# Kernel optimization log

Hardware: AMD Instinct MI355X
Metric: run time of the kernel (lower is better)

Reference implementation:

```python
import jax, jax.numpy as jnp
import numpy as np

EPS = 1e-9
TOP_K = 2


def setup_inputs() -> dict:
    key = jax.random.key(0)
    k = jax.random.split(key, 6)
    B, E, D_IN, D_MODEL, D_SEL = 16384, 8, 900, 512, 128
    return {
        "cycle_curve_data": jax.random.normal(k[0], (B, D_IN), jnp.float32),
        "logits": jax.random.normal(k[1], (B, E), jnp.float32),
        "moe_masks": jax.random.randint(k[2], (B, E), 0, 2, jnp.int32),
        "selection_embeddings": jax.random.normal(k[3], (B, E, D_SEL), jnp.float32),
        "W": jax.random.normal(k[4], (E, D_IN, D_MODEL), jnp.float32) / np.sqrt(D_IN).astype(np.float32),
        "b": jnp.zeros((E, D_MODEL), jnp.float32),
    }


def reference(cycle_curve_data, logits, moe_masks, selection_embeddings, W, b):
    B, E = logits.shape
    mask = (moe_masks == 1).astype(logits.dtype)  # [B, E]
    raw = jax.nn.softmax(logits, axis=1)          # [B, E]

    # inactive-expert mixture for selection embedding
    inactive = raw * (1.0 - mask)
    inactive = inactive / (jnp.sum(inactive, axis=1, keepdims=True) + EPS)
    selection_embedding = jnp.einsum("bes,be->bs", selection_embeddings, inactive)

    # active gates + top-k selection + renormalization
    active = raw * mask
    _, idx = jax.lax.top_k(active, TOP_K)                                  # [B, K]
    top_mask = jnp.sum(jax.nn.one_hot(idx, E, dtype=active.dtype), axis=1)  # [B, E]
    gates = active * top_mask
    gates = gates / (jnp.sum(gates, axis=1, keepdims=True) + EPS)

    # dense formulation of dispatch -> per-expert Linear -> weighted combine:
    # out[b] = sum_e gates[b,e] * (x[b] @ W[e] + b[e])
    expert_out = jnp.einsum("bd,edm->bem", cycle_curve_data, W) + b  # [B, E, D_model]
    final_out = jnp.einsum("bem,be->bm", expert_out, gates).astype(jnp.bfloat16)

    # guide loss (training-mode auxiliary loss)
    s = jnp.sum(raw * mask) / B
    guide_loss = (1.0 - s) * (1.0 - s)
    return final_out, guide_loss, selection_embedding
```

## Files before the change

kernel.cpp:

```cpp
#include <hip/hip_runtime.h>
#include <hip/hip_bf16.h>


#define B_ROWS 16384
#define DIN 900
#define DM 512
#define DSEL 128
#define KP 928
#define NKS 29
#define MAXT 192
#define EPSF 1e-9f

#define OUT_GUIDE (B_ROWS*DM)
#define OUT_SEL   (B_ROWS*DM + 1)

#define WS_COUNTS 0
#define WS_PART   512
#define WS_NT     768
#define WS_OFF    1024
#define WS_ENT    2048
#define WS_BB     9216
#define WS_PIDLR  25600
#define WS_GATEB  91136
#define WS_W8     222208
#define WS_ROWSS  746496
#define WS_WT     812032

typedef __attribute__((ext_vector_type(8))) short short8;
typedef __attribute__((ext_vector_type(8))) unsigned short ushort8;
typedef __attribute__((ext_vector_type(4))) float floatx4;

__device__ inline unsigned short f2bf(float v){
  union { __hip_bfloat16 h; unsigned short u; } c;
  c.h = __float2bfloat16(v);
  return c.u;
}
__device__ inline float bf2f(unsigned short u){
  union { unsigned int i; float f; } c;
  c.i = ((unsigned int)u) << 16;
  return c.f;
}

__global__ __launch_bounds__(256) void cvtw_k(const float* __restrict__ W,
                                              unsigned short* __restrict__ wt){
  __shared__ unsigned short tl[64][65];
  int kt = blockIdx.x, ntb = blockIdx.y, e = blockIdx.z;
  int c = threadIdx.x & 63, q = threadIdx.x >> 6;
  for (int i = 0; i < 16; i++){
    int kl = q + i*4;
    int k = kt*64 + kl;
    float v = (k < DIN) ? W[((size_t)e*DIN + k)*DM + ntb*64 + c] : 0.f;
    tl[kl][c] = f2bf(v);
  }
  __syncthreads();
  for (int i = 0; i < 16; i++){
    int nl = q + i*4;
    int k = kt*64 + c;
    if (k < KP)
      wt[((size_t)e*DM + ntb*64 + nl)*KP + k] = tl[c][nl];
  }
}

__global__ __launch_bounds__(256) void gating_k(const float* __restrict__ logits,
                                                const int* __restrict__ masks,
                                                int* __restrict__ counts,
                                                float* __restrict__ partials,
                                                int* __restrict__ pidlr,
                                                float2* __restrict__ gatesb,
                                                float* __restrict__ w8,
                                                int* __restrict__ blockbase){
  __shared__ int hist[64];
  __shared__ float wsum[4];
  int t = threadIdx.x;
  if (t < 64) hist[t] = 0;
  __syncthreads();
  int b = blockIdx.x*256 + t;
  float4 l0 = *(const float4*)&logits[(size_t)b*8];
  float4 l1 = *(const float4*)&logits[(size_t)b*8 + 4];
  int4  m0 = *(const int4*)&masks[(size_t)b*8];
  int4  m1 = *(const int4*)&masks[(size_t)b*8 + 4];
  float raw[8] = {l0.x,l0.y,l0.z,l0.w,l1.x,l1.y,l1.z,l1.w};
  int   mk[8]  = {m0.x,m0.y,m0.z,m0.w,m1.x,m1.y,m1.z,m1.w};
  float mx = raw[0];
  for (int e = 1; e < 8; e++) mx = fmaxf(mx, raw[e]);
  float Z = 0.f;
  for (int e = 0; e < 8; e++){ raw[e] = expf(raw[e]-mx); Z += raw[e]; }
  float invZ = 1.f/Z;
  float act[8], ina[8]; float srm = 0.f, isum = 0.f;
  for (int e = 0; e < 8; e++){
    raw[e] *= invZ;
    if (mk[e] == 1){ act[e] = raw[e]; ina[e] = 0.f; srm += raw[e]; }
    else           { act[e] = 0.f;    ina[e] = raw[e]; isum += raw[e]; }
  }
  float v1 = -1.f, v2 = -1.f; int e1 = 0, e2 = 0;
  for (int e = 0; e < 8; e++){
    float a = act[e];
    if (a > v1){ v2 = v1; e2 = e1; v1 = a; e1 = e; }
    else if (a > v2){ v2 = a; e2 = e; }
  }
  float den = v1 + v2 + EPSF;
  float g1 = v1/den, g2 = v2/den;
  int lo, hi; float gl, gh;
  if (e1 < e2){ lo = e1; hi = e2; gl = g1; gh = g2; }
  else        { lo = e2; hi = e1; gl = g2; gh = g1; }
  int pid = lo*8 + hi;
  float invI = 1.f/(isum + EPSF);
  for (int e = 0; e < 8; e++) w8[(size_t)b*8 + e] = ina[e]*invI;
  gatesb[b] = make_float2(gl, gh);
  int lr = atomicAdd(&hist[pid], 1);
  pidlr[b] = pid | (lr << 8);
  float s = srm;
  for (int sft = 32; sft > 0; sft >>= 1) s += __shfl_down(s, sft, 64);
  if ((t & 63) == 0) wsum[t >> 6] = s;
  __syncthreads();
  if (t < 64){
    int c = hist[t];
    int base = 0;
    if (c > 0) base = atomicAdd(&counts[t], c);
    blockbase[blockIdx.x*64 + t] = base;
  }
  if (t == 0) partials[blockIdx.x] = wsum[0] + wsum[1] + wsum[2] + wsum[3];
}

__global__ __launch_bounds__(256) void selemb_k(const float* __restrict__ sel,
                                                const float* __restrict__ w8,
                                                float* __restrict__ out){
  int t = threadIdx.x;
  int b = blockIdx.x*2 + (t >> 7);
  int d = t & 127;
  const float* wr = w8 + (size_t)b*8;
  const float* sb = sel + (size_t)b*(8*DSEL);
  float a = 0.f;
  for (int e = 0; e < 8; e++) a += wr[e] * sb[e*DSEL + d];
  out[OUT_SEL + (size_t)b*DSEL + d] = a;
}

__global__ void worklist_k(const int* __restrict__ counts,
                           const float* __restrict__ partials,
                           int* __restrict__ off, int* __restrict__ ntp,
                           int4* __restrict__ entries,
                           float* __restrict__ out){
  int lane = threadIdx.x;
  int c = counts[lane];
  int sc = c;
  for (int s = 1; s < 64; s <<= 1){ int v = __shfl_up(sc, s, 64); if (lane >= s) sc += v; }
  int offp = sc - c;
  off[lane] = offp;
  int nt = (c + 127) >> 7;
  int snt = nt;
  for (int s = 1; s < 64; s <<= 1){ int v = __shfl_up(snt, s, 64); if (lane >= s) snt += v; }
  int tbase = snt - nt;
  int elo = lane >> 3, ehi = lane & 7;
  for (int j = 0; j < nt; ++j){
    int nr = c - j*128; if (nr > 128) nr = 128;
    entries[tbase + j] = make_int4(elo, ehi, offp + j*128, nr);
  }
  int tot = __shfl(snt, 63, 64);
  if (lane == 0) *ntp = tot;
  float p = partials[lane];
  for (int s = 32; s > 0; s >>= 1) p += __shfl_down(p, s, 64);
  if (lane == 0){
    float sv = p * (1.f/B_ROWS);
    float d = 1.f - sv;
    out[OUT_GUIDE] = d*d;
  }
}

__global__ __launch_bounds__(256) void scatter_k(const int* __restrict__ pidlr,
                                                 const int* __restrict__ off,
                                                 const int* __restrict__ blockbase,
                                                 int* __restrict__ rows_s){
  int b = blockIdx.x*256 + threadIdx.x;
  int pl = pidlr[b];
  int p = pl & 255; p &= 63;
  int lr = pl >> 8;
  rows_s[off[p] + blockbase[(b >> 8)*64 + p] + lr] = b;
}

__global__ __launch_bounds__(256) void gemm_k(const float* __restrict__ xf,
                                              const unsigned short* __restrict__ wt,
                                              const float* __restrict__ bias,
                                              const int* __restrict__ ntp,
                                              const int4* __restrict__ entries,
                                              const int* __restrict__ rows_s,
                                              const float2* __restrict__ gatesb,
                                              float* __restrict__ out){
  int tile = blockIdx.x;
  if (tile >= *ntp) return;
  int4 ent = entries[tile];
  int elo = ent.x, ehi = ent.y, start = ent.z, nrows = ent.w;

  __shared__ __align__(16) unsigned short xs[128*40];
  __shared__ int   gidx_s[128];
  __shared__ float glo_s[128];
  __shared__ float ghi_s[128];

  int t = threadIdx.x;
  if (t < 128){
    if (t < nrows){
      int g = rows_s[start + t];
      gidx_s[t] = g;
      float2 gg = gatesb[g];
      glo_s[t] = gg.x; ghi_s[t] = gg.y;
    } else { gidx_s[t] = -1; glo_s[t] = 0.f; ghi_s[t] = 0.f; }
  }
  __syncthreads();

  int lane = t & 63, wid = t >> 6;
  int wrow = wid >> 1, wcol = wid & 1;
  int quad = lane >> 4, l16 = lane & 15;
  int colbase = blockIdx.y*128 + wcol*64;

  int srow = t >> 1, skc = t & 1;
  int sg = gidx_s[srow];
  const float* xrow = xf + (size_t)(sg >= 0 ? sg : 0)*DIN + skc*16;

  floatx4 acc[4][4];
  for (int i = 0; i < 4; i++) for (int j = 0; j < 4; j++)
    for (int r = 0; r < 4; r++) acc[i][j][r] = 0.f;

  for (int pass = 0; pass < 2; ++pass){
    int e = pass ? ehi : elo;
    float g = (sg >= 0) ? (pass ? ghi_s[srow] : glo_s[srow]) : 0.f;
    const unsigned short* wb = wt + (size_t)e*DM*KP;
    for (int ks = 0; ks < NKS; ++ks){
      __syncthreads();
      ushort8 y0, y1;
      if (ks < 28){
        const float4* p = (const float4*)(xrow + ks*32);
        float4 a0 = p[0], a1 = p[1], a2 = p[2], a3 = p[3];
        y0[0]=f2bf(g*a0.x); y0[1]=f2bf(g*a0.y); y0[2]=f2bf(g*a0.z); y0[3]=f2bf(g*a0.w);
        y0[4]=f2bf(g*a1.x); y0[5]=f2bf(g*a1.y); y0[6]=f2bf(g*a1.z); y0[7]=f2bf(g*a1.w);
        y1[0]=f2bf(g*a2.x); y1[1]=f2bf(g*a2.y); y1[2]=f2bf(g*a2.z); y1[3]=f2bf(g*a2.w);
        y1[4]=f2bf(g*a3.x); y1[5]=f2bf(g*a3.y); y1[6]=f2bf(g*a3.z); y1[7]=f2bf(g*a3.w);
      } else {
        for (int j = 0; j < 8; j++){
          int k = ks*32 + skc*16 + j;
          float v = (k < DIN) ? xrow[ks*32 + j] : 0.f;
          y0[j] = f2bf(g*v);
        }
        for (int j = 0; j < 8; j++){
          int k = ks*32 + skc*16 + 8 + j;
          float v = (k < DIN) ? xrow[ks*32 + 8 + j] : 0.f;
          y1[j] = f2bf(g*v);
        }
      }
      *((ushort8*)&xs[srow*40 + skc*16])     = y0;
      *((ushort8*)&xs[srow*40 + skc*16 + 8]) = y1;
      __syncthreads();
      short8 af[4];
      for (int mt = 0; mt < 4; ++mt)
        af[mt] = *((const short8*)&xs[(wrow*64 + mt*16 + l16)*40 + quad*8]);
      for (int nt = 0; nt < 4; ++nt){
        int n = colbase + nt*16 + l16;
        short8 bfr = *((const short8*)(wb + (size_t)n*KP + ks*32 + quad*8));
        for (int mt = 0; mt < 4; ++mt)
          acc[mt][nt] = __builtin_amdgcn_mfma_f32_16x16x32_bf16(af[mt], bfr, acc[mt][nt], 0, 0, 0);
      }
    }
  }
  for (int nt = 0; nt < 4; ++nt){
    int n = colbase + nt*16 + l16;
    float blo = bias[elo*DM + n];
    float bhi = bias[ehi*DM + n];
    for (int mt = 0; mt < 4; ++mt){
      int rl = wrow*64 + mt*16 + quad*4;
      for (int r = 0; r < 4; ++r){
        int rr = rl + r;
        int grow = gidx_s[rr];
        if (grow >= 0){
          float v = acc[mt][nt][r] + glo_s[rr]*blo + ghi_s[rr]*bhi;
          out[(size_t)grow*DM + n] = bf2f(f2bf(v));
        }
      }
    }
  }
}

extern "C" void kernel_launch(void* const* d_in, const int* in_sizes, int n_in,
                              void* d_out, int out_size, void* d_ws, size_t ws_size,
                              hipStream_t stream){
  const float* x      = (const float*)d_in[0];
  const float* logits = (const float*)d_in[1];
  const int*   masks  = (const int*)d_in[2];
  const float* sel    = (const float*)d_in[3];
  const float* W      = (const float*)d_in[4];
  const float* bias   = (const float*)d_in[5];
  float* out = (float*)d_out;
  char* ws = (char*)d_ws;
  int*    counts   = (int*)(ws + WS_COUNTS);
  float*  partials = (float*)(ws + WS_PART);
  int*    ntp      = (int*)(ws + WS_NT);
  int*    off      = (int*)(ws + WS_OFF);
  int4*   entries  = (int4*)(ws + WS_ENT);
  int*    blockbase= (int*)(ws + WS_BB);
  int*    pidlr    = (int*)(ws + WS_PIDLR);
  float2* gatesb   = (float2*)(ws + WS_GATEB);
  float*  w8       = (float*)(ws + WS_W8);
  int*    rows_s   = (int*)(ws + WS_ROWSS);
  unsigned short* wt = (unsigned short*)(ws + WS_WT);

  hipMemsetAsync(ws, 0, 256, stream);
  cvtw_k<<<dim3(15, 8, 8), 256, 0, stream>>>(W, wt);
  gating_k<<<B_ROWS/256, 256, 0, stream>>>(logits, masks, counts, partials, pidlr, gatesb, w8, blockbase);
  worklist_k<<<1, 64, 0, stream>>>(counts, partials, off, ntp, entries, out);
  scatter_k<<<B_ROWS/256, 256, 0, stream>>>(pidlr, off, blockbase, rows_s);
  selemb_k<<<B_ROWS/2, 256, 0, stream>>>(sel, w8, out);
  gemm_k<<<dim3(MAXT, 4), 256, 0, stream>>>(x, wt, bias, ntp, entries, rows_s, gatesb, out);
}
```

Baseline: 326.1 us.

## Double-buffer GEMM A tile, merge expert passes, fold scatter into selemb

The GEMM now loads and converts the x tile once per k-step for both experts, keeping two accumulator sets and applying the gates in the epilogue instead of pre-scaling x. The next k-step's x tile is prefetched into a second LDS buffer, which removes one barrier per iteration. The scatter kernel is folded into the selection-embedding kernel to save a launch, and launch bounds are set to request two blocks per CU. Doubling the accumulators (128 floats per thread) raises register pressure and may cause spills or lower occupancy.

```diff
diff --git a/kernel.cpp b/kernel.cpp
--- a/kernel.cpp
+++ b/kernel.cpp
@@ -124,10 +124,20 @@
 
 __global__ __launch_bounds__(256) void selemb_k(const float* __restrict__ sel,
                                                 const float* __restrict__ w8,
+                                                const int* __restrict__ pidlr,
+                                                const int* __restrict__ off,
+                                                const int* __restrict__ blockbase,
+                                                int* __restrict__ rows_s,
                                                 float* __restrict__ out){
   int t = threadIdx.x;
   int b = blockIdx.x*2 + (t >> 7);
   int d = t & 127;
+  if (d == 0){
+    int pl = pidlr[b];
+    int p = pl & 63;
+    int lr = pl >> 8;
+    rows_s[off[p] + blockbase[(b >> 8)*64 + p] + lr] = b;
+  }
   const float* wr = w8 + (size_t)b*8;
   const float* sb = sel + (size_t)b*(8*DSEL);
   float a = 0.f;
@@ -166,18 +176,7 @@
   }
 }
 
-__global__ __launch_bounds__(256) void scatter_k(const int* __restrict__ pidlr,
-                                                 const int* __restrict__ off,
-                                                 const int* __restrict__ blockbase,
-                                                 int* __restrict__ rows_s){
-  int b = blockIdx.x*256 + threadIdx.x;
-  int pl = pidlr[b];
-  int p = pl & 255; p &= 63;
-  int lr = pl >> 8;
-  rows_s[off[p] + blockbase[(b >> 8)*64 + p] + lr] = b;
-}
-
-__global__ __launch_bounds__(256) void gemm_k(const float* __restrict__ xf,
+__global__ __launch_bounds__(256, 2) void gemm_k(const float* __restrict__ xf,
                                               const unsigned short* __restrict__ wt,
                                               const float* __restrict__ bias,
                                               const int* __restrict__ ntp,
@@ -190,7 +189,7 @@
   int4 ent = entries[tile];
   int elo = ent.x, ehi = ent.y, start = ent.z, nrows = ent.w;
 
-  __shared__ __align__(16) unsigned short xs[128*40];
+  __shared__ __align__(16) unsigned short xs[2][128*40];
   __shared__ int   gidx_s[128];
   __shared__ float glo_s[128];
   __shared__ float ghi_s[128];
@@ -215,50 +214,73 @@
   int sg = gidx_s[srow];
   const float* xrow = xf + (size_t)(sg >= 0 ? sg : 0)*DIN + skc*16;
 
-  floatx4 acc[4][4];
-  for (int i = 0; i < 4; i++) for (int j = 0; j < 4; j++)
-    for (int r = 0; r < 4; r++) acc[i][j][r] = 0.f;
-
-  for (int pass = 0; pass < 2; ++pass){
-    int e = pass ? ehi : elo;
-    float g = (sg >= 0) ? (pass ? ghi_s[srow] : glo_s[srow]) : 0.f;
-    const unsigned short* wb = wt + (size_t)e*DM*KP;
-    for (int ks = 0; ks < NKS; ++ks){
-      __syncthreads();
-      ushort8 y0, y1;
-      if (ks < 28){
-        const float4* p = (const float4*)(xrow + ks*32);
-        float4 a0 = p[0], a1 = p[1], a2 = p[2], a3 = p[3];
-        y0[0]=f2bf(g*a0.x); y0[1]=f2bf(g*a0.y); y0[2]=f2bf(g*a0.z); y0[3]=f2bf(g*a0.w);
-        y0[4]=f2bf(g*a1.x); y0[5]=f2bf(g*a1.y); y0[6]=f2bf(g*a1.z); y0[7]=f2bf(g*a1.w);
-        y1[0]=f2bf(g*a2.x); y1[1]=f2bf(g*a2.y); y1[2]=f2bf(g*a2.z); y1[3]=f2bf(g*a2.w);
-        y1[4]=f2bf(g*a3.x); y1[5]=f2bf(g*a3.y); y1[6]=f2bf(g*a3.z); y1[7]=f2bf(g*a3.w);
+  const unsigned short* wb0 = wt + (size_t)elo*DM*KP;
+  const unsigned short* wb1 = wt + (size_t)ehi*DM*KP;
+
+  floatx4 acc[2][4][4];
+  for (int i = 0; i < 2; i++) for (int j = 0; j < 4; j++) for (int k = 0; k < 4; k++)
+    for (int r = 0; r < 4; r++) acc[i][j][k][r] = 0.f;
+
+  {
+    const float4* p = (const float4*)(xrow);
+    float4 a0 = p[0], a1 = p[1], a2 = p[2], a3 = p[3];
+    ushort8 y0, y1;
+    y0[0]=f2bf(a0.x); y0[1]=f2bf(a0.y); y0[2]=f2bf(a0.z); y0[3]=f2bf(a0.w);
+    y0[4]=f2bf(a1.x); y0[5]=f2bf(a1.y); y0[6]=f2bf(a1.z); y0[7]=f2bf(a1.w);
+    y1[0]=f2bf(a2.x); y1[1]=f2bf(a2.y); y1[2]=f2bf(a2.z); y1[3]=f2bf(a2.w);
+    y1[4]=f2bf(a3.x); y1[5]=f2bf(a3.y); y1[6]=f2bf(a3.z); y1[7]=f2bf(a3.w);
+    *((ushort8*)&xs[0][srow*40 + skc*16])     = y0;
+    *((ushort8*)&xs[0][srow*40 + skc*16 + 8]) = y1;
+  }
+
+  for (int ks = 0; ks < NKS; ++ks){
+    __syncthreads();
+    int cur = ks & 1;
+    int nks = ks + 1;
+
+    float4 b0, b1, b2, b3;
+    if (nks < NKS){
+      if (nks < 28){
+        const float4* p = (const float4*)(xrow + nks*32);
+        b0 = p[0]; b1 = p[1]; b2 = p[2]; b3 = p[3];
       } else {
-        for (int j = 0; j < 8; j++){
-          int k = ks*32 + skc*16 + j;
-          float v = (k < DIN) ? xrow[ks*32 + j] : 0.f;
-          y0[j] = f2bf(g*v);
+        float tmp[16];
+        for (int j = 0; j < 16; j++){
+          int k = nks*32 + skc*16 + j;
+          tmp[j] = (k < DIN) ? xrow[nks*32 + j] : 0.f;
         }
-        for (int j = 0; j < 8; j++){
-          int k = ks*32 + skc*16 + 8 + j;
-          float v = (k < DIN) ? xrow[ks*32 + 8 + j] : 0.f;
-          y1[j] = f2bf(g*v);
-        }
-      }
-      *((ushort8*)&xs[srow*40 + skc*16])     = y0;
-      *((ushort8*)&xs[srow*40 + skc*16 + 8]) = y1;
-      __syncthreads();
-      short8 af[4];
-      for (int mt = 0; mt < 4; ++mt)
-        af[mt] = *((const short8*)&xs[(wrow*64 + mt*16 + l16)*40 + quad*8]);
-      for (int nt = 0; nt < 4; ++nt){
-        int n = colbase + nt*16 + l16;
-        short8 bfr = *((const short8*)(wb + (size_t)n*KP + ks*32 + quad*8));
-        for (int mt = 0; mt < 4; ++mt)
-          acc[mt][nt] = __builtin_amdgcn_mfma_f32_16x16x32_bf16(af[mt], bfr, acc[mt][nt], 0, 0, 0);
+        b0 = make_float4(tmp[0],tmp[1],tmp[2],tmp[3]);
+        b1 = make_float4(tmp[4],tmp[5],tmp[6],tmp[7]);
+        b2 = make_float4(tmp[8],tmp[9],tmp[10],tmp[11]);
+        b3 = make_float4(tmp[12],tmp[13],tmp[14],tmp[15]);
       }
     }
-  }
+
+    short8 af[4];
+    for (int mt = 0; mt < 4; ++mt)
+      af[mt] = *((const short8*)&xs[cur][(wrow*64 + mt*16 + l16)*40 + quad*8]);
+
+    for (int nt = 0; nt < 4; ++nt){
+      int n = colbase + nt*16 + l16;
+      short8 bf0 = *((const short8*)(wb0 + (size_t)n*KP + ks*32 + quad*8));
+      short8 bf1 = *((const short8*)(wb1 + (size_t)n*KP + ks*32 + quad*8));
+      for (int mt = 0; mt < 4; ++mt)
+        acc[0][mt][nt] = __builtin_amdgcn_mfma_f32_16x16x32_bf16(af[mt], bf0, acc[0][mt][nt], 0, 0, 0);
+      for (int mt = 0; mt < 4; ++mt)
+        acc[1][mt][nt] = __builtin_amdgcn_mfma_f32_16x16x32_bf16(af[mt], bf1, acc[1][mt][nt], 0, 0, 0);
+    }
+
+    if (nks < NKS){
+      ushort8 y0, y1;
+      y0[0]=f2bf(b0.x); y0[1]=f2bf(b0.y); y0[2]=f2bf(b0.z); y0[3]=f2bf(b0.w);
+      y0[4]=f2bf(b1.x); y0[5]=f2bf(b1.y); y0[6]=f2bf(b1.z); y0[7]=f2bf(b1.w);
+      y1[0]=f2bf(b2.x); y1[1]=f2bf(b2.y); y1[2]=f2bf(b2.z); y1[3]=f2bf(b2.w);
+      y1[4]=f2bf(b3.x); y1[5]=f2bf(b3.y); y1[6]=f2bf(b3.z); y1[7]=f2bf(b3.w);
+      *((ushort8*)&xs[cur^1][srow*40 + skc*16])     = y0;
+      *((ushort8*)&xs[cur^1][srow*40 + skc*16 + 8]) = y1;
+    }
+  }
+
   for (int nt = 0; nt < 4; ++nt){
     int n = colbase + nt*16 + l16;
     float blo = bias[elo*DM + n];
@@ -269,7 +291,7 @@
         int rr = rl + r;
         int grow = gidx_s[rr];
         if (grow >= 0){
-          float v = acc[mt][nt][r] + glo_s[rr]*blo + ghi_s[rr]*bhi;
+          float v = glo_s[rr]*(acc[0][mt][nt][r] + blo) + ghi_s[rr]*(acc[1][mt][nt][r] + bhi);
           out[(size_t)grow*DM + n] = bf2f(f2bf(v));
         }
       }
@@ -304,7 +326,6 @@
   cvtw_k<<<dim3(15, 8, 8), 256, 0, stream>>>(W, wt);
   gating_k<<<B_ROWS/256, 256, 0, stream>>>(logits, masks, counts, partials, pidlr, gatesb, w8, blockbase);
   worklist_k<<<1, 64, 0, stream>>>(counts, partials, off, ntp, entries, out);
-  scatter_k<<<B_ROWS/256, 256, 0, stream>>>(pidlr, off, blockbase, rows_s);
-  selemb_k<<<B_ROWS/2, 256, 0, stream>>>(sel, w8, out);
+  selemb_k<<<B_ROWS/2, 256, 0, stream>>>(sel, w8, pidlr, off, blockbase, rows_s, out);
   gemm_k<<<dim3(MAXT, 4), 256, 0, stream>>>(x, wt, bias, ntp, entries, rows_s, gatesb, out);
 }
```

Result: slower. 340.4 us (+4.4%).
